# Optimization experiments

Measured on AMD Instinct MI355X. Metric: run time of the kernel, lower is better.

## Reference

```python
import jax, jax.numpy as jnp
import numpy as np

EPS = 1e-6


def _build_cayley():
    # Blade ordering of the CEGNN CliffordAlgebra for Cl(3,0): combinations order
    # 1, e1, e2, e3, e12, e13, e23, e123. Metric (1,1,1) => e_k^2 = +1.
    blades = [(), (0,), (1,), (2,), (0, 1), (0, 2), (1, 2), (0, 1, 2)]
    index = {b: i for i, b in enumerate(blades)}
    cayley = np.zeros((8, 8, 8), dtype=np.float32)
    for i, a in enumerate(blades):
        for j, b in enumerate(blades):
            arr = list(a) + list(b)
            sign = 1
            # bubble sort, counting transpositions of anticommuting generators
            for p in range(len(arr)):
                for q in range(len(arr) - 1):
                    if arr[q] > arr[q + 1]:
                        arr[q], arr[q + 1] = arr[q + 1], arr[q]
                        sign = -sign
            # contract equal adjacent generators (e_k e_k = +1)
            out = []
            q = 0
            while q < len(arr):
                if q + 1 < len(arr) and arr[q] == arr[q + 1]:
                    q += 2
                else:
                    out.append(arr[q])
                    q += 1
            cayley[i, j, index[tuple(out)]] = sign
    return cayley


_CAYLEY = jnp.asarray(_build_cayley())  # (8, 8, 8)


def _mvlinear(x, W, b):
    # MVLinear(subspaces=False): channel mixing shared across blades,
    # bias embedded into the scalar (grade-0) blade only.
    y = jnp.einsum("bmi,nm->bni", x, W)
    return y.at[:, :, 0].add(b)


def setup_inputs() -> dict:
    key = jax.random.key(0)
    ks = jax.random.split(key, 7)
    B, Cin, Ch, Cout = 16384, 512, 512, 512
    s = 1.0 / np.sqrt(Cin)
    return {
        "vec1": jax.random.normal(ks[0], (B, Cin, 8), dtype=jnp.float32),
        "W_left": jax.random.normal(ks[1], (Ch, Cin), dtype=jnp.float32) * s,
        "b_left": jax.random.normal(ks[2], (Ch,), dtype=jnp.float32) * 0.01,
        "W_right": jax.random.normal(ks[3], (Ch, Cin), dtype=jnp.float32) * s,
        "b_right": jax.random.normal(ks[4], (Ch,), dtype=jnp.float32) * 0.01,
        "W_out": jax.random.normal(ks[5], (Cout, Ch), dtype=jnp.float32) * s,
        "b_out": jax.random.normal(ks[6], (Cout,), dtype=jnp.float32) * 0.01,
        "a_norm": jnp.ones((Cout,), dtype=jnp.float32),
    }


def reference(vec1, W_left, b_left, W_right, b_right, W_out, b_out, a_norm):
    vec_right = _mvlinear(vec1, W_right, b_right)   # (B, Ch, 8)
    vec_left = _mvlinear(vec1, W_left, b_left)      # (B, Ch, 8)
    # geometric product via the sparse Cayley table of Cl(3,0)
    gp = jnp.einsum("bmi,ijk,bmj->bmk", vec_left, _CAYLEY, vec_right)
    out = _mvlinear(gp, W_out, b_out)               # (B, Cout, 8)
    # MVLayerNorm: per-multivector quadratic-form norm (all-positive metric =>
    # sqrt of sum of squared blade coefficients), averaged over channels.
    norm = jnp.sqrt(jnp.sum(out * out, axis=-1, keepdims=True))  # (B, Cout, 1)
    norm = jnp.mean(norm, axis=1, keepdims=True) + EPS           # (B, 1, 1)
    return a_norm[None, :, None] * out / norm
```

## Files before the change

kernel.cpp:

```cpp
#include <hip/hip_runtime.h>
#include <cstdint>
#include <cstddef>

typedef _Float16 f16;
typedef __attribute__((ext_vector_type(8))) _Float16 f16x8;
typedef __attribute__((ext_vector_type(4))) _Float16 f16x4;
typedef __attribute__((ext_vector_type(4))) float f32x4;

#define MFMA_F16(a, b, c) __builtin_amdgcn_mfma_f32_16x16x32_f16((a), (b), (c), 0, 0, 0)

#define GL2LDS(gsrc, ldst)                                                  \
    __builtin_amdgcn_global_load_lds(                                        \
        (const __attribute__((address_space(1))) void*)(gsrc),               \
        (__attribute__((address_space(3))) void*)(ldst), 16, 0, 0)

#define SWZ(row) (((row) >> 1) & 3)


__global__ __launch_bounds__(256) void k0(const float* __restrict__ x,
                                          const float* __restrict__ wl,
                                          const float* __restrict__ wr,
                                          const float* __restrict__ wo,
                                          f16* __restrict__ wdst,
                                          f16* __restrict__ xt) {
    const int bid = blockIdx.x;
    if (bid >= 8192) {
        int i = (bid - 8192) * 256 + threadIdx.x;
        wdst[i]          = (f16)wl[i];
        wdst[262144 + i] = (f16)wr[i];
        wdst[524288 + i] = (f16)wo[i];
        return;
    }
    const int b = (bid >> 1) * 4 + (threadIdx.x >> 6);
    const int m = (bid & 1) * 256 + (threadIdx.x & 63) * 4;
    const float* src = x + ((size_t)b * 512 + m) * 8;
    f32x4 v[8];
#pragma unroll
    for (int u = 0; u < 8; ++u) v[u] = *(const f32x4*)(src + u * 4);
#pragma unroll
    for (int i = 0; i < 8; ++i) {
        f16x4 w;
#pragma unroll
        for (int j = 0; j < 4; ++j) w[j] = (f16)v[j * 2 + (i >> 2)][i & 3];
        *(f16x4*)(xt + (size_t)i * 8388608 + (size_t)b * 512 + m) = w;
    }
}

__global__ __launch_bounds__(512, 4) void k1(
    const f16* __restrict__ xt, const f16* __restrict__ wf,
    const float* __restrict__ bl_p, const float* __restrict__ br_p,
    char* gp_out)
{
    __shared__ __align__(16) f16 AsF[2 * 8192];
    __shared__ __align__(16) f16 WsF[2 * 4096];

    const int L = blockIdx.x;
    const int xcd = L & 7, sl = L >> 3;
    const int bt = xcd * 64 + (sl >> 3), ct = sl & 7;
    const int b0 = bt * 32, n0 = ct * 64;

    const int tid = threadIdx.x, lane = tid & 63, wv = tid >> 6;
    const int wb = wv >> 2, wn = wv & 3;
    const int r_lo = lane & 15, s_hi = lane >> 4;

    const int gA0 = tid, gA1 = tid + 512;
    const int ba0 = gA0 >> 7, ra0 = (gA0 >> 2) & 31, ga0 = (gA0 & 3) ^ SWZ(ra0);
    const int ba1 = gA1 >> 7, ra1 = (gA1 >> 2) & 31, ga1 = (gA1 & 3) ^ SWZ(ra1);
    const f16* aS0 = xt + (size_t)ba0 * 8388608 + (size_t)(b0 + ra0) * 512 + ga0 * 8;
    const f16* aS1 = xt + (size_t)ba1 * 8388608 + (size_t)(b0 + ra1) * 512 + ga1 * 8;
    const int side = tid >> 8, wn_ = (tid >> 2) & 63, wg = (tid & 3) ^ SWZ(wn_);
    const f16* wS = wf + (size_t)side * 262144 + (size_t)(n0 + wn_) * 512 + wg * 8;

    f16* aD0 = AsF + wv * 512;
    f16* aD1 = AsF + 4096 + wv * 512;
    f16* wD  = WsF + wv * 512;

    const int ar = wb * 16 + r_lo;
    const int aoff = ar * 32 + ((s_hi ^ SWZ(ar)) << 3);
    const int nloc = wn * 16 + r_lo;
    const int boff = nloc * 32 + ((s_hi ^ SWZ(nloc)) << 3);

    f32x4 accL[8], accR[8];
    const f32x4 zero = {0.f, 0.f, 0.f, 0.f};
#pragma unroll
    for (int i = 0; i < 8; ++i) { accL[i] = zero; accR[i] = zero; }

    GL2LDS(aS0, aD0);
    GL2LDS(aS1, aD1);
    GL2LDS(wS, wD);
    __syncthreads();

    for (int kk = 0; kk < 16; ++kk) {
        const int buf = kk & 1;
        if (kk < 15) {
            const int nb = (buf ^ 1);
            GL2LDS(aS0 + (kk + 1) * 32, aD0 + nb * 8192);
            GL2LDS(aS1 + (kk + 1) * 32, aD1 + nb * 8192);
            GL2LDS(wS + (kk + 1) * 32, wD + nb * 4096);
        }
        const f16* Ab = AsF + buf * 8192;
        const f16* Wb = WsF + buf * 4096;
        f16x8 bL = *(const f16x8*)(Wb + boff);
        f16x8 bR = *(const f16x8*)(Wb + 2048 + boff);
#pragma unroll
        for (int i = 0; i < 8; ++i) {
            f16x8 a = *(const f16x8*)(Ab + i * 1024 + aoff);
            accL[i] = MFMA_F16(a, bL, accL[i]);
            accR[i] = MFMA_F16(a, bR, accR[i]);
        }
        __syncthreads();
    }

    const int n_g = n0 + nloc;
    const float blv = bl_p[n_g], brv = br_p[n_g];
#pragma unroll
    for (int rr = 0; rr < 4; ++rr) {
        const int b_g = b0 + wb * 16 + s_hi * 4 + rr;
        float Lv[8], Rv[8];
#pragma unroll
        for (int i = 0; i < 8; ++i) { Lv[i] = accL[i][rr]; Rv[i] = accR[i][rr]; }
        Lv[0] += blv; Rv[0] += brv;
        float g[8];
        g[0] = Lv[0]*Rv[0]+Lv[1]*Rv[1]+Lv[2]*Rv[2]+Lv[3]*Rv[3]-Lv[4]*Rv[4]-Lv[5]*Rv[5]-Lv[6]*Rv[6]-Lv[7]*Rv[7];
        g[1] = Lv[0]*Rv[1]+Lv[1]*Rv[0]-Lv[2]*Rv[4]-Lv[3]*Rv[5]+Lv[4]*Rv[2]+Lv[5]*Rv[3]-Lv[6]*Rv[7]-Lv[7]*Rv[6];
        g[2] = Lv[0]*Rv[2]+Lv[1]*Rv[4]+Lv[2]*Rv[0]-Lv[3]*Rv[6]-Lv[4]*Rv[1]+Lv[5]*Rv[7]+Lv[6]*Rv[3]+Lv[7]*Rv[5];
        g[3] = Lv[0]*Rv[3]+Lv[1]*Rv[5]+Lv[2]*Rv[6]+Lv[3]*Rv[0]-Lv[4]*Rv[7]-Lv[5]*Rv[1]-Lv[6]*Rv[2]-Lv[7]*Rv[4];
        g[4] = Lv[0]*Rv[4]+Lv[1]*Rv[2]-Lv[2]*Rv[1]+Lv[3]*Rv[7]+Lv[4]*Rv[0]-Lv[5]*Rv[6]+Lv[6]*Rv[5]+Lv[7]*Rv[3];
        g[5] = Lv[0]*Rv[5]+Lv[1]*Rv[3]-Lv[2]*Rv[7]-Lv[3]*Rv[1]+Lv[4]*Rv[6]+Lv[5]*Rv[0]-Lv[6]*Rv[4]-Lv[7]*Rv[2];
        g[6] = Lv[0]*Rv[6]+Lv[1]*Rv[7]+Lv[2]*Rv[3]-Lv[3]*Rv[2]-Lv[4]*Rv[5]+Lv[5]*Rv[4]+Lv[6]*Rv[0]+Lv[7]*Rv[1];
        g[7] = Lv[0]*Rv[7]+Lv[1]*Rv[6]-Lv[2]*Rv[5]+Lv[3]*Rv[4]+Lv[4]*Rv[3]-Lv[5]*Rv[2]+Lv[6]*Rv[1]+Lv[7]*Rv[0];
        char* dst = gp_out + (size_t)b_g * 16384 + (size_t)n_g * 2;
#pragma unroll
        for (int i = 0; i < 8; ++i) *(f16*)(dst + (size_t)i * 1024) = (f16)g[i];
    }
}

__global__ __launch_bounds__(1024, 4) void k2(
    const char* gp_in, const f16* __restrict__ wo,
    const float* __restrict__ bo_p, const float* __restrict__ an_p,
    float* outp)
{
    __shared__ __align__(16) f16 AsF[2 * 4096];
    __shared__ __align__(16) f16 BsF[2 * 16384];
    __shared__ float red[16][16];

    const int b0 = blockIdx.x * 16;
    const int tid = threadIdx.x, lane = tid & 63, wv = tid >> 6;
    const int r_lo = lane & 15, s_hi = lane >> 4;

    const int gA = tid;
    const int abl = gA >> 6, arw = (gA >> 2) & 15, agp = (gA & 3) ^ SWZ(arw);
    const char* aS = gp_in + (size_t)(b0 + arw) * 16384 + abl * 1024 + agp * 16;
    const int gB0 = tid, gB1 = tid + 1024;
    const int bn0 = gB0 >> 2, bg0 = (gB0 & 3) ^ SWZ(bn0);
    const int bn1 = gB1 >> 2, bg1 = (gB1 & 3) ^ SWZ(bn1);
    const f16* bS0 = wo + (size_t)bn0 * 512 + bg0 * 8;
    const f16* bS1 = wo + (size_t)bn1 * 512 + bg1 * 8;

    f16* aD  = AsF + wv * 512;
    f16* bD0 = BsF + wv * 512;
    f16* bD1 = BsF + 8192 + wv * 512;

    const int aoff = r_lo * 32 + ((s_hi ^ SWZ(r_lo)) << 3);
    const int nl0 = wv * 32 + r_lo, nl1 = nl0 + 16;
    const int boff0 = nl0 * 32 + ((s_hi ^ SWZ(nl0)) << 3);
    const int boff1 = nl1 * 32 + ((s_hi ^ SWZ(nl1)) << 3);

    f32x4 acc[2][8];
    const f32x4 zero = {0.f, 0.f, 0.f, 0.f};
#pragma unroll
    for (int st = 0; st < 2; ++st)
#pragma unroll
        for (int i = 0; i < 8; ++i) acc[st][i] = zero;

    if (wv < 8) GL2LDS(aS, aD);
    GL2LDS(bS0, bD0);
    GL2LDS(bS1, bD1);
    __syncthreads();

    for (int kk = 0; kk < 16; ++kk) {
        const int buf = kk & 1;
        if (kk < 15) {
            const int nb = buf ^ 1;
            if (wv < 8) GL2LDS(aS + (kk + 1) * 64, aD + nb * 4096);
            GL2LDS(bS0 + (kk + 1) * 32, bD0 + nb * 16384);
            GL2LDS(bS1 + (kk + 1) * 32, bD1 + nb * 16384);
        }
        const f16* Ab = AsF + buf * 4096;
        const f16* Bb = BsF + buf * 16384;
        f16x8 bf0 = *(const f16x8*)(Bb + boff0);
        f16x8 bf1 = *(const f16x8*)(Bb + boff1);
#pragma unroll
        for (int i = 0; i < 8; ++i) {
            f16x8 a = *(const f16x8*)(Ab + i * 512 + aoff);
            acc[0][i] = MFMA_F16(a, bf0, acc[0][i]);
            acc[1][i] = MFMA_F16(a, bf1, acc[1][i]);
        }
        __syncthreads();
    }

    const float bo0 = bo_p[nl0], bo1 = bo_p[nl1];
    const float an0 = an_p[nl0], an1 = an_p[nl1];

    float partial[4];
#pragma unroll
    for (int rr = 0; rr < 4; ++rr) {
        float o = acc[0][0][rr] + bo0;
        float ss = o * o;
#pragma unroll
        for (int i = 1; i < 8; ++i) ss += acc[0][i][rr] * acc[0][i][rr];
        float s = sqrtf(ss);
        o = acc[1][0][rr] + bo1;
        ss = o * o;
#pragma unroll
        for (int i = 1; i < 8; ++i) ss += acc[1][i][rr] * acc[1][i][rr];
        partial[rr] = s + sqrtf(ss);
    }
#pragma unroll
    for (int off = 1; off < 16; off <<= 1)
#pragma unroll
        for (int rr = 0; rr < 4; ++rr) partial[rr] += __shfl_xor(partial[rr], off);
    if (r_lo == 0)
#pragma unroll
        for (int rr = 0; rr < 4; ++rr) red[s_hi * 4 + rr][wv] = partial[rr];
    __syncthreads();

#pragma unroll
    for (int rr = 0; rr < 4; ++rr) {
        float tot = 0.f;
#pragma unroll
        for (int w = 0; w < 16; ++w) tot += red[s_hi * 4 + rr][w];
        const float inv = 1.0f / (tot * (1.0f / 512.0f) + 1e-6f);
        const float sc0 = an0 * inv, sc1 = an1 * inv;
        const int b_g = b0 + s_hi * 4 + rr;
        float* dst = outp + (size_t)b_g * 4096;
        f32x4 v;
        v[0] = (acc[0][0][rr] + bo0) * sc0;
        v[1] = acc[0][1][rr] * sc0; v[2] = acc[0][2][rr] * sc0; v[3] = acc[0][3][rr] * sc0;
        *(f32x4*)(dst + (size_t)nl0 * 8) = v;
        v[0] = acc[0][4][rr] * sc0; v[1] = acc[0][5][rr] * sc0;
        v[2] = acc[0][6][rr] * sc0; v[3] = acc[0][7][rr] * sc0;
        *(f32x4*)(dst + (size_t)nl0 * 8 + 4) = v;
        v[0] = (acc[1][0][rr] + bo1) * sc1;
        v[1] = acc[1][1][rr] * sc1; v[2] = acc[1][2][rr] * sc1; v[3] = acc[1][3][rr] * sc1;
        *(f32x4*)(dst + (size_t)nl1 * 8) = v;
        v[0] = acc[1][4][rr] * sc1; v[1] = acc[1][5][rr] * sc1;
        v[2] = acc[1][6][rr] * sc1; v[3] = acc[1][7][rr] * sc1;
        *(f32x4*)(dst + (size_t)nl1 * 8 + 4) = v;
    }
}

extern "C" void kernel_launch(void* const* d_in, const int* in_sizes, int n_in,
                              void* d_out, int out_size, void* d_ws, size_t ws_size,
                              hipStream_t stream) {
    const float* x  = (const float*)d_in[0];
    const float* wl = (const float*)d_in[1];
    const float* bl = (const float*)d_in[2];
    const float* wr = (const float*)d_in[3];
    const float* br = (const float*)d_in[4];
    const float* wo = (const float*)d_in[5];
    const float* bo = (const float*)d_in[6];
    const float* an = (const float*)d_in[7];
    f16* wf = (f16*)d_ws;
    f16* xt = wf + (1 << 20);

    hipLaunchKernelGGL(k0, dim3(9216), dim3(256), 0, stream, x, wl, wr, wo, wf, xt);
    hipLaunchKernelGGL(k1, dim3(4096), dim3(512), 0, stream, xt, wf, bl, br, (char*)d_out);
    hipLaunchKernelGGL(k2, dim3(1024), dim3(1024), 0, stream,
                       (const char*)d_out, wf + 524288, bo, an, (float*)d_out);
}
```

Measured before the change: 447.0 us.

## Triple-buffer GEMM stages with vmcnt waits and widen k2 per-wave tiles

Both GEMM kernels move from a double-buffered LDS pipeline with __syncthreads to a three-stage ring. Loads run two k-tiles ahead, with explicit s_waitcnt vmcnt counts and raw barriers, so global-to-LDS copies overlap more of the MFMA work. k2 is also restructured from 16 waves to 8 waves, each computing four 16-column output tiles instead of two. That doubles per-wave register accumulators and B-fragment reuse. Launch-bound occupancy hints drop, trading occupancy for deeper pipelining and more registers, at some risk of lower latency hiding.

Result: faster. 432.4 us (-3.3%).

```diff
diff --git a/kernel.cpp b/kernel.cpp
--- a/kernel.cpp
+++ b/kernel.cpp
@@ -13,6 +13,9 @@
     __builtin_amdgcn_global_load_lds(                                        \
         (const __attribute__((address_space(1))) void*)(gsrc),               \
         (__attribute__((address_space(3))) void*)(ldst), 16, 0, 0)
+
+#define WAITV(n) asm volatile("s_waitcnt vmcnt(" #n ")" ::: "memory")
+#define BAR() __builtin_amdgcn_s_barrier()
 
 #define SWZ(row) (((row) >> 1) & 3)
 
@@ -46,13 +49,13 @@
     }
 }
 
-__global__ __launch_bounds__(512, 4) void k1(
+__global__ __launch_bounds__(512, 2) void k1(
     const f16* __restrict__ xt, const f16* __restrict__ wf,
     const float* __restrict__ bl_p, const float* __restrict__ br_p,
     char* gp_out)
 {
-    __shared__ __align__(16) f16 AsF[2 * 8192];
-    __shared__ __align__(16) f16 WsF[2 * 4096];
+    __shared__ __align__(16) f16 AsF[3 * 8192];
+    __shared__ __align__(16) f16 WsF[3 * 4096];
 
     const int L = blockIdx.x;
     const int xcd = L & 7, sl = L >> 3;
@@ -85,21 +88,24 @@
 #pragma unroll
     for (int i = 0; i < 8; ++i) { accL[i] = zero; accR[i] = zero; }
 
-    GL2LDS(aS0, aD0);
-    GL2LDS(aS1, aD1);
-    GL2LDS(wS, wD);
-    __syncthreads();
-
+    auto stage = [&](int kt, int buf) {
+        GL2LDS(aS0 + kt * 32, aD0 + buf * 8192);
+        GL2LDS(aS1 + kt * 32, aD1 + buf * 8192);
+        GL2LDS(wS + kt * 32, wD + buf * 4096);
+    };
+
+    stage(0, 0);
+    stage(1, 1);
+
+#pragma unroll
     for (int kk = 0; kk < 16; ++kk) {
-        const int buf = kk & 1;
-        if (kk < 15) {
-            const int nb = (buf ^ 1);
-            GL2LDS(aS0 + (kk + 1) * 32, aD0 + nb * 8192);
-            GL2LDS(aS1 + (kk + 1) * 32, aD1 + nb * 8192);
-            GL2LDS(wS + (kk + 1) * 32, wD + nb * 4096);
-        }
-        const f16* Ab = AsF + buf * 8192;
-        const f16* Wb = WsF + buf * 4096;
+        if (kk + 2 < 16) stage(kk + 2, (kk + 2) % 3);
+        if (kk <= 13)      { WAITV(6); }
+        else if (kk == 14) { WAITV(3); }
+        else               { WAITV(0); }
+        BAR();
+        const f16* Ab = AsF + (kk % 3) * 8192;
+        const f16* Wb = WsF + (kk % 3) * 4096;
         f16x8 bL = *(const f16x8*)(Wb + boff);
         f16x8 bR = *(const f16x8*)(Wb + 2048 + boff);
 #pragma unroll
@@ -108,7 +114,7 @@
             accL[i] = MFMA_F16(a, bL, accL[i]);
             accR[i] = MFMA_F16(a, bR, accR[i]);
         }
-        __syncthreads();
+        BAR();
     }
 
     const int n_g = n0 + nloc;
@@ -135,86 +141,100 @@
     }
 }
 
-__global__ __launch_bounds__(1024, 4) void k2(
+__global__ __launch_bounds__(512, 1) void k2(
     const char* gp_in, const f16* __restrict__ wo,
     const float* __restrict__ bo_p, const float* __restrict__ an_p,
     float* outp)
 {
-    __shared__ __align__(16) f16 AsF[2 * 4096];
-    __shared__ __align__(16) f16 BsF[2 * 16384];
-    __shared__ float red[16][16];
+    __shared__ __align__(16) f16 AsF[3 * 4096];
+    __shared__ __align__(16) f16 BsF[3 * 16384];
+    __shared__ float red[16][8];
 
     const int b0 = blockIdx.x * 16;
     const int tid = threadIdx.x, lane = tid & 63, wv = tid >> 6;
     const int r_lo = lane & 15, s_hi = lane >> 4;
 
-    const int gA = tid;
-    const int abl = gA >> 6, arw = (gA >> 2) & 15, agp = (gA & 3) ^ SWZ(arw);
+    const int abl = tid >> 6, arw = (tid >> 2) & 15, agp = (tid & 3) ^ SWZ(arw);
     const char* aS = gp_in + (size_t)(b0 + arw) * 16384 + abl * 1024 + agp * 16;
-    const int gB0 = tid, gB1 = tid + 1024;
-    const int bn0 = gB0 >> 2, bg0 = (gB0 & 3) ^ SWZ(bn0);
-    const int bn1 = gB1 >> 2, bg1 = (gB1 & 3) ^ SWZ(bn1);
-    const f16* bS0 = wo + (size_t)bn0 * 512 + bg0 * 8;
-    const f16* bS1 = wo + (size_t)bn1 * 512 + bg1 * 8;
-
-    f16* aD  = AsF + wv * 512;
-    f16* bD0 = BsF + wv * 512;
-    f16* bD1 = BsF + 8192 + wv * 512;
+    const f16* bS[4];
+#pragma unroll
+    for (int j = 0; j < 4; ++j) {
+        const int g = j * 512 + tid;
+        const int bn = g >> 2, bg = (g & 3) ^ SWZ(bn);
+        bS[j] = wo + (size_t)bn * 512 + bg * 8;
+    }
+
+    f16* aD = AsF + wv * 512;
+    f16* bD = BsF + wv * 512;
 
     const int aoff = r_lo * 32 + ((s_hi ^ SWZ(r_lo)) << 3);
-    const int nl0 = wv * 32 + r_lo, nl1 = nl0 + 16;
-    const int boff0 = nl0 * 32 + ((s_hi ^ SWZ(nl0)) << 3);
-    const int boff1 = nl1 * 32 + ((s_hi ^ SWZ(nl1)) << 3);
-
-    f32x4 acc[2][8];
+    int boffs[4];
+#pragma unroll
+    for (int t = 0; t < 4; ++t) {
+        const int nl = wv * 64 + t * 16 + r_lo;
+        boffs[t] = nl * 32 + ((s_hi ^ SWZ(nl)) << 3);
+    }
+
+    f32x4 acc[4][8];
     const f32x4 zero = {0.f, 0.f, 0.f, 0.f};
 #pragma unroll
-    for (int st = 0; st < 2; ++st)
-#pragma unroll
-        for (int i = 0; i < 8; ++i) acc[st][i] = zero;
-
-    if (wv < 8) GL2LDS(aS, aD);
-    GL2LDS(bS0, bD0);
-    GL2LDS(bS1, bD1);
-    __syncthreads();
-
+    for (int t = 0; t < 4; ++t)
+#pragma unroll
+        for (int i = 0; i < 8; ++i) acc[t][i] = zero;
+
+    auto stage = [&](int kt, int buf) {
+        GL2LDS(aS + kt * 64, aD + buf * 4096);
+#pragma unroll
+        for (int j = 0; j < 4; ++j)
+            GL2LDS(bS[j] + kt * 32, bD + buf * 16384 + j * 4096);
+    };
+
+    stage(0, 0);
+    stage(1, 1);
+
+#pragma unroll
     for (int kk = 0; kk < 16; ++kk) {
-        const int buf = kk & 1;
-        if (kk < 15) {
-            const int nb = buf ^ 1;
-            if (wv < 8) GL2LDS(aS + (kk + 1) * 64, aD + nb * 4096);
-            GL2LDS(bS0 + (kk + 1) * 32, bD0 + nb * 16384);
-            GL2LDS(bS1 + (kk + 1) * 32, bD1 + nb * 16384);
-        }
-        const f16* Ab = AsF + buf * 4096;
-        const f16* Bb = BsF + buf * 16384;
-        f16x8 bf0 = *(const f16x8*)(Bb + boff0);
-        f16x8 bf1 = *(const f16x8*)(Bb + boff1);
+        if (kk + 2 < 16) stage(kk + 2, (kk + 2) % 3);
+        if (kk <= 13)      { WAITV(10); }
+        else if (kk == 14) { WAITV(5); }
+        else               { WAITV(0); }
+        BAR();
+        const f16* Ab = AsF + (kk % 3) * 4096;
+        const f16* Bb = BsF + (kk % 3) * 16384;
+        f16x8 bf[4];
+#pragma unroll
+        for (int t = 0; t < 4; ++t) bf[t] = *(const f16x8*)(Bb + boffs[t]);
 #pragma unroll
         for (int i = 0; i < 8; ++i) {
             f16x8 a = *(const f16x8*)(Ab + i * 512 + aoff);
-            acc[0][i] = MFMA_F16(a, bf0, acc[0][i]);
-            acc[1][i] = MFMA_F16(a, bf1, acc[1][i]);
-        }
-        __syncthreads();
-    }
-
-    const float bo0 = bo_p[nl0], bo1 = bo_p[nl1];
-    const float an0 = an_p[nl0], an1 = an_p[nl1];
+            acc[0][i] = MFMA_F16(a, bf[0], acc[0][i]);
+            acc[1][i] = MFMA_F16(a, bf[1], acc[1][i]);
+            acc[2][i] = MFMA_F16(a, bf[2], acc[2][i]);
+            acc[3][i] = MFMA_F16(a, bf[3], acc[3][i]);
+        }
+        BAR();
+    }
+
+    float bo_t[4], an_t[4];
+#pragma unroll
+    for (int t = 0; t < 4; ++t) {
+        const int c = wv * 64 + t * 16 + r_lo;
+        bo_t[t] = bo_p[c]; an_t[t] = an_p[c];
+    }
 
     float partial[4];
 #pragma unroll
     for (int rr = 0; rr < 4; ++rr) {
-        float o = acc[0][0][rr] + bo0;
-        float ss = o * o;
-#pragma unroll
-        for (int i = 1; i < 8; ++i) ss += acc[0][i][rr] * acc[0][i][rr];
-        float s = sqrtf(ss);
-        o = acc[1][0][rr] + bo1;
-        ss = o * o;
-#pragma unroll
-        for (int i = 1; i < 8; ++i) ss += acc[1][i][rr] * acc[1][i][rr];
-        partial[rr] = s + sqrtf(ss);
+        float sum = 0.f;
+#pragma unroll
+        for (int t = 0; t < 4; ++t) {
+            float o = acc[t][0][rr] + bo_t[t];
+            float ss = o * o;
+#pragma unroll
+            for (int i = 1; i < 8; ++i) ss += acc[t][i][rr] * acc[t][i][rr];
+            sum += sqrtf(ss);
+        }
+        partial[rr] = sum;
     }
 #pragma unroll
     for (int off = 1; off < 16; off <<= 1)
@@ -229,24 +249,22 @@
     for (int rr = 0; rr < 4; ++rr) {
         float tot = 0.f;
 #pragma unroll
-        for (int w = 0; w < 16; ++w) tot += red[s_hi * 4 + rr][w];
+        for (int w = 0; w < 8; ++w) tot += red[s_hi * 4 + rr][w];
         const float inv = 1.0f / (tot * (1.0f / 512.0f) + 1e-6f);
-        const float sc0 = an0 * inv, sc1 = an1 * inv;
         const int b_g = b0 + s_hi * 4 + rr;
         float* dst = outp + (size_t)b_g * 4096;
-        f32x4 v;
-        v[0] = (acc[0][0][rr] + bo0) * sc0;
-        v[1] = acc[0][1][rr] * sc0; v[2] = acc[0][2][rr] * sc0; v[3] = acc[0][3][rr] * sc0;
-        *(f32x4*)(dst + (size_t)nl0 * 8) = v;
-        v[0] = acc[0][4][rr] * sc0; v[1] = acc[0][5][rr] * sc0;
-        v[2] = acc[0][6][rr] * sc0; v[3] = acc[0][7][rr] * sc0;
-        *(f32x4*)(dst + (size_t)nl0 * 8 + 4) = v;
-        v[0] = (acc[1][0][rr] + bo1) * sc1;
-        v[1] = acc[1][1][rr] * sc1; v[2] = acc[1][2][rr] * sc1; v[3] = acc[1][3][rr] * sc1;
-        *(f32x4*)(dst + (size_t)nl1 * 8) = v;
-        v[0] = acc[1][4][rr] * sc1; v[1] = acc[1][5][rr] * sc1;
-        v[2] = acc[1][6][rr] * sc1; v[3] = acc[1][7][rr] * sc1;
-        *(f32x4*)(dst + (size_t)nl1 * 8 + 4) = v;
+#pragma unroll
+        for (int t = 0; t < 4; ++t) {
+            const float sc = an_t[t] * inv;
+            const int c = wv * 64 + t * 16 + r_lo;
+            f32x4 v0, v1;
+            v0[0] = (acc[t][0][rr] + bo_t[t]) * sc;
+            v0[1] = acc[t][1][rr] * sc; v0[2] = acc[t][2][rr] * sc; v0[3] = acc[t][3][rr] * sc;
+            v1[0] = acc[t][4][rr] * sc; v1[1] = acc[t][5][rr] * sc;
+            v1[2] = acc[t][6][rr] * sc; v1[3] = acc[t][7][rr] * sc;
+            *(f32x4*)(dst + (size_t)c * 8) = v0;
+            *(f32x4*)(dst + (size_t)c * 8 + 4) = v1;
+        }
     }
 }
 
@@ -266,6 +284,6 @@
 
     hipLaunchKernelGGL(k0, dim3(9216), dim3(256), 0, stream, x, wl, wr, wo, wf, xt);
     hipLaunchKernelGGL(k1, dim3(4096), dim3(512), 0, stream, xt, wf, bl, br, (char*)d_out);
-    hipLaunchKernelGGL(k2, dim3(1024), dim3(1024), 0, stream,
+    hipLaunchKernelGGL(k2, dim3(1024), dim3(512), 0, stream,
                        (const char*)d_out, wf + 524288, bo, an, (float*)d_out);
 }
```

## Triple-buffer LDS staging with explicit vmcnt waits and widen k1 tiles

Applied to the files above, without the earlier changes.

Both GEMM kernels move from double to triple buffering. They prefetch two K-tiles ahead and replace the __syncthreads pairs with explicit s_waitcnt vmcnt counts plus raw barriers, so global-to-LDS loads can overlap more compute. k1 also doubles its block to 1024 threads with 128 output channels per block, halving the grid and reusing each staged x tile across more channels. The cost is more LDS per block (k1 now 96KB), which may limit occupancy. The hand-tuned vmcnt counts are fragile and depend on how the compiler orders the loads.

Measured after the change: 445.8 us. Within noise of the previous version (-0.3%).

```diff
diff --git a/kernel.cpp b/kernel.cpp
--- a/kernel.cpp
+++ b/kernel.cpp
@@ -13,6 +13,9 @@
     __builtin_amdgcn_global_load_lds(                                        \
         (const __attribute__((address_space(1))) void*)(gsrc),               \
         (__attribute__((address_space(3))) void*)(ldst), 16, 0, 0)
+
+#define WAITV(n) asm volatile("s_waitcnt vmcnt(" #n ")" ::: "memory")
+#define BAR() __builtin_amdgcn_s_barrier()
 
 #define SWZ(row) (((row) >> 1) & 3)
 
@@ -46,34 +49,30 @@
     }
 }
 
-__global__ __launch_bounds__(512, 4) void k1(
+__global__ __launch_bounds__(1024, 4) void k1(
     const f16* __restrict__ xt, const f16* __restrict__ wf,
     const float* __restrict__ bl_p, const float* __restrict__ br_p,
     char* gp_out)
 {
-    __shared__ __align__(16) f16 AsF[2 * 8192];
-    __shared__ __align__(16) f16 WsF[2 * 4096];
+    __shared__ __align__(16) f16 AsF[3 * 8192];
+    __shared__ __align__(16) f16 WsF[3 * 8192];
 
     const int L = blockIdx.x;
     const int xcd = L & 7, sl = L >> 3;
-    const int bt = xcd * 64 + (sl >> 3), ct = sl & 7;
-    const int b0 = bt * 32, n0 = ct * 64;
+    const int bt = xcd * 64 + (sl >> 2), ct = sl & 3;
+    const int b0 = bt * 32, n0 = ct * 128;
 
     const int tid = threadIdx.x, lane = tid & 63, wv = tid >> 6;
-    const int wb = wv >> 2, wn = wv & 3;
+    const int wb = wv >> 3, wn = wv & 7;
     const int r_lo = lane & 15, s_hi = lane >> 4;
 
-    const int gA0 = tid, gA1 = tid + 512;
-    const int ba0 = gA0 >> 7, ra0 = (gA0 >> 2) & 31, ga0 = (gA0 & 3) ^ SWZ(ra0);
-    const int ba1 = gA1 >> 7, ra1 = (gA1 >> 2) & 31, ga1 = (gA1 & 3) ^ SWZ(ra1);
-    const f16* aS0 = xt + (size_t)ba0 * 8388608 + (size_t)(b0 + ra0) * 512 + ga0 * 8;
-    const f16* aS1 = xt + (size_t)ba1 * 8388608 + (size_t)(b0 + ra1) * 512 + ga1 * 8;
-    const int side = tid >> 8, wn_ = (tid >> 2) & 63, wg = (tid & 3) ^ SWZ(wn_);
-    const f16* wS = wf + (size_t)side * 262144 + (size_t)(n0 + wn_) * 512 + wg * 8;
-
-    f16* aD0 = AsF + wv * 512;
-    f16* aD1 = AsF + 4096 + wv * 512;
-    f16* wD  = WsF + wv * 512;
+    const int ab = tid >> 7, arw = (tid >> 2) & 31, ac = (tid & 3) ^ SWZ(arw);
+    const f16* aS = xt + (size_t)ab * 8388608 + (size_t)(b0 + arw) * 512 + ac * 8;
+    const int wsd = tid >> 9, wnr = (tid >> 2) & 127, wc = (tid & 3) ^ SWZ(wnr);
+    const f16* wS = wf + (size_t)wsd * 262144 + (size_t)(n0 + wnr) * 512 + wc * 8;
+
+    f16* aD = AsF + wv * 512;
+    f16* wD = WsF + wv * 512;
 
     const int ar = wb * 16 + r_lo;
     const int aoff = ar * 32 + ((s_hi ^ SWZ(ar)) << 3);
@@ -85,30 +84,32 @@
 #pragma unroll
     for (int i = 0; i < 8; ++i) { accL[i] = zero; accR[i] = zero; }
 
-    GL2LDS(aS0, aD0);
-    GL2LDS(aS1, aD1);
-    GL2LDS(wS, wD);
-    __syncthreads();
-
+    auto stage = [&](int kt, int buf) {
+        GL2LDS(aS + kt * 32, aD + buf * 8192);
+        GL2LDS(wS + kt * 32, wD + buf * 8192);
+    };
+
+    stage(0, 0);
+    stage(1, 1);
+
+#pragma unroll
     for (int kk = 0; kk < 16; ++kk) {
-        const int buf = kk & 1;
-        if (kk < 15) {
-            const int nb = (buf ^ 1);
-            GL2LDS(aS0 + (kk + 1) * 32, aD0 + nb * 8192);
-            GL2LDS(aS1 + (kk + 1) * 32, aD1 + nb * 8192);
-            GL2LDS(wS + (kk + 1) * 32, wD + nb * 4096);
-        }
-        const f16* Ab = AsF + buf * 8192;
-        const f16* Wb = WsF + buf * 4096;
+        if (kk + 2 < 16) stage(kk + 2, (kk + 2) % 3);
+        if (kk <= 13)      { WAITV(4); }
+        else if (kk == 14) { WAITV(2); }
+        else               { WAITV(0); }
+        BAR();
+        const f16* Ab = AsF + (kk % 3) * 8192;
+        const f16* Wb = WsF + (kk % 3) * 8192;
         f16x8 bL = *(const f16x8*)(Wb + boff);
-        f16x8 bR = *(const f16x8*)(Wb + 2048 + boff);
+        f16x8 bR = *(const f16x8*)(Wb + 4096 + boff);
 #pragma unroll
         for (int i = 0; i < 8; ++i) {
             f16x8 a = *(const f16x8*)(Ab + i * 1024 + aoff);
             accL[i] = MFMA_F16(a, bL, accL[i]);
             accR[i] = MFMA_F16(a, bR, accR[i]);
         }
-        __syncthreads();
+        BAR();
     }
 
     const int n_g = n0 + nloc;
@@ -140,22 +141,19 @@
     const float* __restrict__ bo_p, const float* __restrict__ an_p,
     float* outp)
 {
-    __shared__ __align__(16) f16 AsF[2 * 4096];
-    __shared__ __align__(16) f16 BsF[2 * 16384];
+    __shared__ __align__(16) f16 AsF[3 * 4096];
+    __shared__ __align__(16) f16 BsF[3 * 16384];
     __shared__ float red[16][16];
 
     const int b0 = blockIdx.x * 16;
     const int tid = threadIdx.x, lane = tid & 63, wv = tid >> 6;
     const int r_lo = lane & 15, s_hi = lane >> 4;
 
-    const int gA = tid;
-    const int abl = gA >> 6, arw = (gA >> 2) & 15, agp = (gA & 3) ^ SWZ(arw);
-    const char* aS = gp_in + (size_t)(b0 + arw) * 16384 + abl * 1024 + agp * 16;
-    const int gB0 = tid, gB1 = tid + 1024;
-    const int bn0 = gB0 >> 2, bg0 = (gB0 & 3) ^ SWZ(bn0);
-    const int bn1 = gB1 >> 2, bg1 = (gB1 & 3) ^ SWZ(bn1);
-    const f16* bS0 = wo + (size_t)bn0 * 512 + bg0 * 8;
-    const f16* bS1 = wo + (size_t)bn1 * 512 + bg1 * 8;
+    const int abl = tid >> 6, arw = (tid >> 2) & 15, agp = (tid & 3) ^ SWZ(arw);
+    const char* aS = gp_in + (size_t)(b0 + arw) * 16384 + (size_t)(abl & 7) * 1024 + agp * 16;
+    const int bn = tid >> 2, bg = (tid & 3) ^ SWZ(bn);
+    const f16* bS0 = wo + (size_t)bn * 512 + bg * 8;
+    const f16* bS1 = wo + (size_t)(bn + 256) * 512 + bg * 8;
 
     f16* aD  = AsF + wv * 512;
     f16* bD0 = BsF + wv * 512;
@@ -173,21 +171,24 @@
 #pragma unroll
         for (int i = 0; i < 8; ++i) acc[st][i] = zero;
 
-    if (wv < 8) GL2LDS(aS, aD);
-    GL2LDS(bS0, bD0);
-    GL2LDS(bS1, bD1);
-    __syncthreads();
-
+    auto stage = [&](int kt, int buf) {
+        if (wv < 8) GL2LDS(aS + kt * 64, aD + buf * 4096);
+        GL2LDS(bS0 + kt * 32, bD0 + buf * 16384);
+        GL2LDS(bS1 + kt * 32, bD1 + buf * 16384);
+    };
+
+    stage(0, 0);
+    stage(1, 1);
+
+#pragma unroll
     for (int kk = 0; kk < 16; ++kk) {
-        const int buf = kk & 1;
-        if (kk < 15) {
-            const int nb = buf ^ 1;
-            if (wv < 8) GL2LDS(aS + (kk + 1) * 64, aD + nb * 4096);
-            GL2LDS(bS0 + (kk + 1) * 32, bD0 + nb * 16384);
-            GL2LDS(bS1 + (kk + 1) * 32, bD1 + nb * 16384);
-        }
-        const f16* Ab = AsF + buf * 4096;
-        const f16* Bb = BsF + buf * 16384;
+        if (kk + 2 < 16) stage(kk + 2, (kk + 2) % 3);
+        if (kk <= 13)      { if (wv < 8) { WAITV(6); } else { WAITV(4); } }
+        else if (kk == 14) { if (wv < 8) { WAITV(3); } else { WAITV(2); } }
+        else               { WAITV(0); }
+        BAR();
+        const f16* Ab = AsF + (kk % 3) * 4096;
+        const f16* Bb = BsF + (kk % 3) * 16384;
         f16x8 bf0 = *(const f16x8*)(Bb + boff0);
         f16x8 bf1 = *(const f16x8*)(Bb + boff1);
 #pragma unroll
@@ -196,7 +197,7 @@
             acc[0][i] = MFMA_F16(a, bf0, acc[0][i]);
             acc[1][i] = MFMA_F16(a, bf1, acc[1][i]);
         }
-        __syncthreads();
+        BAR();
     }
 
     const float bo0 = bo_p[nl0], bo1 = bo_p[nl1];
@@ -265,7 +266,7 @@
     f16* xt = wf + (1 << 20);
 
     hipLaunchKernelGGL(k0, dim3(9216), dim3(256), 0, stream, x, wl, wr, wo, wf, xt);
-    hipLaunchKernelGGL(k1, dim3(4096), dim3(512), 0, stream, xt, wf, bl, br, (char*)d_out);
+    hipLaunchKernelGGL(k1, dim3(2048), dim3(1024), 0, stream, xt, wf, bl, br, (char*)d_out);
     hipLaunchKernelGGL(k2, dim3(1024), dim3(1024), 0, stream,
                        (const char*)d_out, wf + 524288, bo, an, (float*)d_out);
 }
```
